# Optimization experiments

Hardware: AMD Instinct MI355X
Metric: run time of the kernel (lower is better)

Reference implementation:

```python
import jax, jax.numpy as jnp
import numpy as np

D_MODEL = 512
NHEAD = 8
DK = D_MODEL // NHEAD
DIM_FF = 2048
LN_EPS = 1e-5


def setup_inputs() -> dict:
    key = jax.random.key(0)
    ks = jax.random.split(key, 12)
    B, L = 8, 1024
    s = 1.0 / np.sqrt(D_MODEL)
    sf = 1.0 / np.sqrt(DIM_FF)
    return {
        "x": jax.random.normal(ks[0], (B, L, D_MODEL), jnp.float32),
        "key_padding_mask": jnp.zeros((B, L), dtype=bool),
        "bias": jax.random.normal(ks[1], (B, L, L), jnp.float32),
        # projection weights stored [in, out] so y = x @ W + b (matches torch Linear math)
        "Wq": jax.random.normal(ks[2], (D_MODEL, D_MODEL), jnp.float32) * s,
        "bq": jnp.zeros((D_MODEL,), jnp.float32),
        "Wk": jax.random.normal(ks[3], (D_MODEL, D_MODEL), jnp.float32) * s,
        "bk": jnp.zeros((D_MODEL,), jnp.float32),
        "Wv": jax.random.normal(ks[4], (D_MODEL, D_MODEL), jnp.float32) * s,
        "bv": jnp.zeros((D_MODEL,), jnp.float32),
        "Wo": jax.random.normal(ks[5], (D_MODEL, D_MODEL), jnp.float32) * s,
        "bo": jnp.zeros((D_MODEL,), jnp.float32),
        "ln1_g": jnp.ones((D_MODEL,), jnp.float32),
        "ln1_b": jnp.zeros((D_MODEL,), jnp.float32),
        "W1": jax.random.normal(ks[6], (D_MODEL, DIM_FF), jnp.float32) * s,
        "b1": jnp.zeros((DIM_FF,), jnp.float32),
        "W2": jax.random.normal(ks[7], (DIM_FF, D_MODEL), jnp.float32) * sf,
        "b2": jnp.zeros((D_MODEL,), jnp.float32),
        "ln2_g": jnp.ones((D_MODEL,), jnp.float32),
        "ln2_b": jnp.zeros((D_MODEL,), jnp.float32),
    }


def _layernorm(x, g, b):
    mu = jnp.mean(x, axis=-1, keepdims=True)
    var = jnp.mean(jnp.square(x - mu), axis=-1, keepdims=True)
    return (x - mu) * jax.lax.rsqrt(var + LN_EPS) * g + b


def reference(x, key_padding_mask, bias, Wq, bq, Wk, bk, Wv, bv, Wo, bo,
              ln1_g, ln1_b, W1, b1, W2, b2, ln2_g, ln2_b):
    B, L, H = x.shape
    residual = x
    # [B, L, D] -> [B, nhead, L, dk]
    q = (x @ Wq + bq).reshape(B, L, NHEAD, DK).transpose(0, 2, 1, 3)
    k = (x @ Wk + bk).reshape(B, L, NHEAD, DK).transpose(0, 2, 1, 3)
    v = (x @ Wv + bv).reshape(B, L, NHEAD, DK).transpose(0, 2, 1, 3)
    scores = jnp.einsum("bhqd,bhkd->bhqk", q, k) / np.sqrt(DK)
    scores = scores + bias[:, None, :, :]
    scores = jnp.where(key_padding_mask[:, None, None, :], -jnp.inf, scores)
    attn = jax.nn.softmax(scores, axis=-1)  # dropout p=0 (eval)
    out = jnp.einsum("bhqk,bhkd->bhqd", attn, v)
    out = out.transpose(0, 2, 1, 3).reshape(B, L, H)
    out = out @ Wo + bo
    x = _layernorm(residual + out, ln1_g, ln1_b)
    residual = x
    h = jax.nn.relu(x @ W1 + b1)
    x = h @ W2 + b2
    return _layernorm(residual + x, ln2_g, ln2_b)
```

## Files before the change

### kernel.cpp

```cpp
#include <hip/hip_runtime.h>
#include <math.h>

#define NHEAD 8
#define DKD 64
#define DMODEL 512
#define LSEQ 1024
#define NBL 8192

typedef __attribute__((ext_vector_type(8))) short bf8;
typedef __attribute__((ext_vector_type(4))) float f4;

__device__ inline unsigned short f2bf(float f) {
    union { float f; unsigned u; } v; v.f = f;
    unsigned r = v.u + 0x7FFFu + ((v.u >> 16) & 1u);
    return (unsigned short)(r >> 16);
}

__device__ __forceinline__ void gload16(const void* g, void* l) {
    __builtin_amdgcn_global_load_lds(
        (const __attribute__((address_space(1))) unsigned int*)g,
        (__attribute__((address_space(3))) unsigned int*)l, 16, 0, 0);
}

__global__ __launch_bounds__(256) void conv_bf16(
    const float* __restrict__ in, unsigned short* __restrict__ out, int n)
{
    int i = (blockIdx.x * 256 + threadIdx.x) * 4;
    if (i >= n) return;
    float4 v = *(const float4*)(in + i);
    ushort4 o;
    o.x = f2bf(v.x); o.y = f2bf(v.y); o.z = f2bf(v.z); o.w = f2bf(v.w);
    *(ushort4*)(out + i) = o;
}

__global__ __launch_bounds__(256) void transpose_bf16(
    const float* __restrict__ W, unsigned short* __restrict__ Wt, int K, int N)
{
    __shared__ float tile[64][65];
    const int k0 = blockIdx.y * 64, n0 = blockIdx.x * 64;
    const int c = threadIdx.x & 63, r0 = (threadIdx.x >> 6) * 16;
    #pragma unroll
    for (int i = 0; i < 16; ++i)
        tile[r0 + i][c] = W[(size_t)(k0 + r0 + i) * N + n0 + c];
    __syncthreads();
    #pragma unroll
    for (int i = 0; i < 16; ++i)
        Wt[(size_t)(n0 + r0 + i) * K + k0 + c] = f2bf(tile[c][r0 + i]);
}

__global__ void concat3(const float* __restrict__ a, const float* __restrict__ b,
                        const float* __restrict__ c, float* __restrict__ o)
{
    int i = blockIdx.x * 256 + threadIdx.x;
    if (i < 512) o[i] = a[i];
    else if (i < 1024) o[i] = b[i - 512];
    else if (i < 1536) o[i] = c[i - 1024];
}

__global__ void maskf_kernel(const unsigned char* __restrict__ m,
                             float* __restrict__ o, int n)
{
    int i = blockIdx.x * 256 + threadIdx.x;
    if (i < n) o[i] = m[i] ? -1e30f : 0.f;
}

__global__ __launch_bounds__(256) void mfma_gemm(
    const unsigned short* __restrict__ A, const unsigned short* __restrict__ Bt,
    const float* __restrict__ bias, const float* __restrict__ resid,
    void* __restrict__ outp, int M, int N, int K, int relu, int outmode,
    unsigned short* __restrict__ qs, unsigned short* __restrict__ ks,
    unsigned short* __restrict__ vts)
{
    __shared__ uint4 As[1024];
    __shared__ uint4 Bs[1024];

    const int t = threadIdx.x;
    const int lane = t & 63, w = t >> 6;
    const int g = lane >> 4, r15 = lane & 15;
    const int wr = w >> 1, wc = w & 1;
    const int rowBase = blockIdx.y * 128, colBase = blockIdx.x * 128;

    f4 acc[4][4] = {};

    const int r  = t >> 3;
    const int chs = (t & 7) ^ (r & 7);
    unsigned short* Al = (unsigned short*)As + (w * 8) * 64;
    unsigned short* Bl = (unsigned short*)Bs + (w * 8) * 64;

    for (int k0 = 0; k0 < K; k0 += 64) {
        __syncthreads();
        {
            const unsigned short* Ag = A  + (size_t)(rowBase + r) * K + k0 + chs * 8;
            const unsigned short* Bg = Bt + (size_t)(colBase + r) * K + k0 + chs * 8;
            #pragma unroll
            for (int p = 0; p < 4; ++p) {
                gload16(Ag + (size_t)(p * 32) * K, Al + p * 32 * 64);
                gload16(Bg + (size_t)(p * 32) * K, Bl + p * 32 * 64);
            }
        }
        __syncthreads();
        #pragma unroll
        for (int kk = 0; kk < 2; ++kk) {
            bf8 af[4], bfr[4];
            #pragma unroll
            for (int m = 0; m < 4; ++m) {
                int ra = wr * 64 + m * 16 + r15;
                af[m] = *(const bf8*)&As[ra * 8 + ((kk * 4 + g) ^ (ra & 7))];
                int rb = wc * 64 + m * 16 + r15;
                bfr[m] = *(const bf8*)&Bs[rb * 8 + ((kk * 4 + g) ^ (rb & 7))];
            }
            #pragma unroll
            for (int m = 0; m < 4; ++m)
                #pragma unroll
                for (int n = 0; n < 4; ++n)
                    acc[m][n] = __builtin_amdgcn_mfma_f32_16x16x32_bf16(
                        af[m], bfr[n], acc[m][n], 0, 0, 0);
        }
    }

    #pragma unroll
    for (int m = 0; m < 4; ++m) {
        #pragma unroll
        for (int n = 0; n < 4; ++n) {
            int col = colBase + wc * 64 + n * 16 + r15;
            float bv = bias[col];
            #pragma unroll
            for (int rr = 0; rr < 4; ++rr) {
                int row = rowBase + wr * 64 + m * 16 + g * 4 + rr;
                float v = acc[m][n][rr] + bv;
                if (relu) v = fmaxf(v, 0.f);
                if (outmode == 0) {
                    size_t idx = (size_t)row * N + col;
                    if (resid) v += resid[idx];
                    ((float*)outp)[idx] = v;
                } else if (outmode == 1) {
                    ((unsigned short*)outp)[(size_t)row * N + col] = f2bf(v);
                } else {
                    int sel = col >> 9, hd = col & 511;
                    int h = hd >> 6, dk = hd & 63;
                    int b = row >> 10, l = row & 1023;
                    unsigned short bw = f2bf(v);
                    size_t bh = (size_t)(b * NHEAD + h);
                    if (sel == 0)      qs[(bh * LSEQ + l) * DKD + dk] = bw;
                    else if (sel == 1) ks[(bh * LSEQ + l) * DKD + dk] = bw;
                    else               vts[(bh * DKD + dk) * LSEQ + l] = bw;
                }
            }
        }
    }
}

__global__ __launch_bounds__(256) void attn_mfma(
    const unsigned short* __restrict__ Qg, const unsigned short* __restrict__ Kg,
    const unsigned short* __restrict__ Vtg, const float* __restrict__ bias,
    const float* __restrict__ maskF, unsigned short* __restrict__ Ob)
{
    __shared__ uint4 Ks[512];
    __shared__ uint4 Vs[512];
    __shared__ unsigned int Pb[2048];

    const int t = threadIdx.x;
    const int lane = t & 63, w = t >> 6;
    const int g = lane >> 4, r15 = lane & 15;

    const int p = blockIdx.x;
    const int logical = (p & 7) * 128 + (p >> 3);
    const int bh = logical >> 4, qt = logical & 15;
    const int b = bh >> 3, h = bh & 7;

    bf8 qf[2];
    const int qrow = qt * 64 + w * 16 + r15;
    {
        const unsigned short* qp = Qg + ((size_t)bh * LSEQ + qrow) * DKD + g * 8;
        qf[0] = *(const bf8*)qp;
        qf[1] = *(const bf8*)(qp + 32);
    }

    float mrun = -1e30f, lsum = 0.f;
    f4 oacc[4] = {};

    const float* biasRow = bias + ((size_t)b << 20) + (size_t)qrow * LSEQ;
    const float* maskFb  = maskF + b * LSEQ;

    const int sr  = t >> 3;
    const int chs = (t & 7) ^ (sr & 7);
    unsigned short* Kl = (unsigned short*)Ks + (w * 8) * 64;
    unsigned short* Vl = (unsigned short*)Vs + (w * 8) * 64;
    unsigned short* Pw = (unsigned short*)&Pb[w * 512];

    for (int kt = 0; kt < 16; ++kt) {
        const int key0 = kt * 64;
        __syncthreads();
        {
            const unsigned short* Kgp = Kg  + ((size_t)bh * LSEQ + key0 + sr) * DKD + chs * 8;
            const unsigned short* Vgp = Vtg + ((size_t)bh * DKD + sr) * LSEQ + key0 + chs * 8;
            gload16(Kgp, Kl);
            gload16(Kgp + (size_t)32 * DKD, Kl + 32 * 64);
            gload16(Vgp, Vl);
            gload16(Vgp + (size_t)32 * LSEQ, Vl + 32 * 64);
        }
        __syncthreads();

        f4 sacc[4] = {};
        #pragma unroll
        for (int kk = 0; kk < 2; ++kk)
            #pragma unroll
            for (int m = 0; m < 4; ++m) {
                int row = m * 16 + r15;
                bf8 kf = *(const bf8*)&Ks[row * 8 + ((kk * 4 + g) ^ (row & 7))];
                sacc[m] = __builtin_amdgcn_mfma_f32_16x16x32_bf16(kf, qf[kk], sacc[m], 0, 0, 0);
            }

        float s[16];
        float pmax = -1e30f;
        #pragma unroll
        for (int m = 0; m < 4; ++m) {
            float4 bv = *(const float4*)(biasRow + key0 + m * 16 + g * 4);
            float4 mv = *(const float4*)(maskFb  + key0 + m * 16 + g * 4);
            const float* bvp = (const float*)&bv;
            const float* mvp = (const float*)&mv;
            #pragma unroll
            for (int j = 0; j < 4; ++j) {
                float sv = fmaf(sacc[m][j], 0.125f, bvp[j] + mvp[j]);
                s[m * 4 + j] = sv;
                pmax = fmaxf(pmax, sv);
            }
        }
        pmax = fmaxf(pmax, __shfl_xor(pmax, 16));
        pmax = fmaxf(pmax, __shfl_xor(pmax, 32));

        if (!__all(pmax <= mrun + 8.f)) {
            float mnew = fmaxf(mrun, pmax);
            float scale = __expf(mrun - mnew);
            lsum *= scale;
            #pragma unroll
            for (int m = 0; m < 4; ++m)
                #pragma unroll
                for (int j = 0; j < 4; ++j) oacc[m][j] *= scale;
            mrun = mnew;
        }

        float psum = 0.f;
        #pragma unroll
        for (int i = 0; i < 16; ++i) { s[i] = __expf(s[i] - mrun); psum += s[i]; }
        psum += __shfl_xor(psum, 16);
        psum += __shfl_xor(psum, 32);
        lsum += psum;

        #pragma unroll
        for (int m = 0; m < 4; ++m) {
            uint2 pk;
            pk.x = (unsigned)f2bf(s[m * 4 + 0]) | ((unsigned)f2bf(s[m * 4 + 1]) << 16);
            pk.y = (unsigned)f2bf(s[m * 4 + 2]) | ((unsigned)f2bf(s[m * 4 + 3]) << 16);
            int off = (r15 * 128 + m * 32 + g * 8) ^ ((r15 & 7) << 4);
            *(uint2*)((char*)Pw + off) = pk;
        }

        #pragma unroll
        for (int kk = 0; kk < 2; ++kk) {
            int off = (r15 * 128 + kk * 64 + g * 16) ^ ((r15 & 7) << 4);
            bf8 pf = *(const bf8*)((char*)Pw + off);
            #pragma unroll
            for (int m = 0; m < 4; ++m) {
                int row = m * 16 + r15;
                bf8 vf = *(const bf8*)&Vs[row * 8 + ((kk * 4 + g) ^ (row & 7))];
                oacc[m] = __builtin_amdgcn_mfma_f32_16x16x32_bf16(vf, pf, oacc[m], 0, 0, 0);
            }
        }
    }

    {
        float inv = 1.f / lsum;
        unsigned short* op = Ob + ((size_t)b * LSEQ + qrow) * DMODEL + h * DKD;
        #pragma unroll
        for (int m = 0; m < 4; ++m) {
            ushort4 o4;
            o4.x = f2bf(oacc[m][0] * inv);
            o4.y = f2bf(oacc[m][1] * inv);
            o4.z = f2bf(oacc[m][2] * inv);
            o4.w = f2bf(oacc[m][3] * inv);
            *(ushort4*)(op + m * 16 + g * 4) = o4;
        }
    }
}

__global__ __launch_bounds__(256) void ln_kernel(
    const float* __restrict__ in, const float* __restrict__ g,
    const float* __restrict__ bt, float* __restrict__ out,
    unsigned short* __restrict__ outb)
{
    const int row  = blockIdx.x * 4 + (threadIdx.x >> 6);
    const int lane = threadIdx.x & 63;
    const float* rp = in + (size_t)row * DMODEL + lane * 8;
    float4 x0 = *(const float4*)rp;
    float4 x1 = *(const float4*)(rp + 4);
    float xs[8] = {x0.x, x0.y, x0.z, x0.w, x1.x, x1.y, x1.z, x1.w};

    float sum = 0.f;
    #pragma unroll
    for (int i = 0; i < 8; ++i) sum += xs[i];
    #pragma unroll
    for (int off = 32; off; off >>= 1) sum += __shfl_xor(sum, off);
    float mu = sum * (1.f / 512.f);

    float vs = 0.f;
    #pragma unroll
    for (int i = 0; i < 8; ++i) { float d = xs[i] - mu; vs += d * d; }
    #pragma unroll
    for (int off = 32; off; off >>= 1) vs += __shfl_xor(vs, off);
    float rs = rsqrtf(vs * (1.f / 512.f) + 1e-5f);

    const float* gp = g  + lane * 8;
    const float* bp = bt + lane * 8;
    float4 g0 = *(const float4*)gp, g1 = *(const float4*)(gp + 4);
    float4 b0 = *(const float4*)bp, b1 = *(const float4*)(bp + 4);
    float gs[8] = {g0.x, g0.y, g0.z, g0.w, g1.x, g1.y, g1.z, g1.w};
    float bs[8] = {b0.x, b0.y, b0.z, b0.w, b1.x, b1.y, b1.z, b1.w};

    float res[8];
    #pragma unroll
    for (int i = 0; i < 8; ++i) res[i] = (xs[i] - mu) * rs * gs[i] + bs[i];

    float* op = out + (size_t)row * DMODEL + lane * 8;
    float4 r0 = {res[0], res[1], res[2], res[3]};
    float4 r1 = {res[4], res[5], res[6], res[7]};
    *(float4*)op       = r0;
    *(float4*)(op + 4) = r1;

    if (outb) {
        unsigned short* ob = outb + (size_t)row * DMODEL + lane * 8;
        ushort4 u0, u1;
        u0.x = f2bf(res[0]); u0.y = f2bf(res[1]); u0.z = f2bf(res[2]); u0.w = f2bf(res[3]);
        u1.x = f2bf(res[4]); u1.y = f2bf(res[5]); u1.z = f2bf(res[6]); u1.w = f2bf(res[7]);
        *(ushort4*)ob       = u0;
        *(ushort4*)(ob + 4) = u1;
    }
}

extern "C" void kernel_launch(void* const* d_in, const int* in_sizes, int n_in,
                              void* d_out, int out_size, void* d_ws, size_t ws_size,
                              hipStream_t stream)
{
    const float*         x    = (const float*)d_in[0];
    const unsigned char* mask = (const unsigned char*)d_in[1];
    const float*         bias = (const float*)d_in[2];
    const float* Wq = (const float*)d_in[3];
    const float* bq = (const float*)d_in[4];
    const float* Wk = (const float*)d_in[5];
    const float* bk = (const float*)d_in[6];
    const float* Wv = (const float*)d_in[7];
    const float* bv = (const float*)d_in[8];
    const float* Wo = (const float*)d_in[9];
    const float* bo = (const float*)d_in[10];
    const float* ln1g = (const float*)d_in[11];
    const float* ln1b = (const float*)d_in[12];
    const float* W1 = (const float*)d_in[13];
    const float* b1 = (const float*)d_in[14];
    const float* W2 = (const float*)d_in[15];
    const float* b2 = (const float*)d_in[16];
    const float* ln2g = (const float*)d_in[17];
    const float* ln2b = (const float*)d_in[18];

    char* W = (char*)d_ws;
    unsigned short* Qb   = (unsigned short*)(W);
    unsigned short* Kb   = (unsigned short*)(W + (8u << 20));
    unsigned short* Vtb  = (unsigned short*)(W + (16u << 20));
    unsigned short* Oball= (unsigned short*)(W + (24u << 20));
    unsigned short* hb   = (unsigned short*)(W);
    float*          y12  = (float*)(W + (32u << 20));
    float*          x1   = (float*)(W + (48u << 20));
    unsigned short* xb   = (unsigned short*)(W + (64u << 20));
    unsigned short* x1b  = xb;
    unsigned short* Wqkv = (unsigned short*)(W + (72u << 20));
    unsigned short* Wot  = (unsigned short*)(W + (74u << 20));
    unsigned short* W1t  = (unsigned short*)(W + (75u << 20));
    unsigned short* W2t  = (unsigned short*)(W + (77u << 20));
    float*          bqkv = (float*)(W + (79u << 20));
    float*          maskF= (float*)(W + (79u << 20) + 65536);
    float*          outp = (float*)d_out;

    conv_bf16<<<dim3(4096), dim3(256), 0, stream>>>(x, xb, NBL * DMODEL);
    transpose_bf16<<<dim3(8, 8),  dim3(256), 0, stream>>>(Wq, Wqkv,          512, 512);
    transpose_bf16<<<dim3(8, 8),  dim3(256), 0, stream>>>(Wk, Wqkv + 262144, 512, 512);
    transpose_bf16<<<dim3(8, 8),  dim3(256), 0, stream>>>(Wv, Wqkv + 524288, 512, 512);
    transpose_bf16<<<dim3(8, 8),  dim3(256), 0, stream>>>(Wo, Wot, 512, 512);
    transpose_bf16<<<dim3(32, 8), dim3(256), 0, stream>>>(W1, W1t, 512, 2048);
    transpose_bf16<<<dim3(8, 32), dim3(256), 0, stream>>>(W2, W2t, 2048, 512);
    concat3<<<dim3(6), dim3(256), 0, stream>>>(bq, bk, bv, bqkv);
    maskf_kernel<<<dim3(32), dim3(256), 0, stream>>>(mask, maskF, NBL);

    mfma_gemm<<<dim3(12, 64), dim3(256), 0, stream>>>(
        xb, Wqkv, bqkv, nullptr, nullptr, NBL, 1536, 512, 0, 2, Qb, Kb, Vtb);

    attn_mfma<<<dim3(1024), dim3(256), 0, stream>>>(Qb, Kb, Vtb, bias, maskF, Oball);

    mfma_gemm<<<dim3(4, 64), dim3(256), 0, stream>>>(
        Oball, Wot, bo, x, y12, NBL, 512, 512, 0, 0, nullptr, nullptr, nullptr);

    ln_kernel<<<dim3(NBL / 4), dim3(256), 0, stream>>>(y12, ln1g, ln1b, x1, x1b);

    mfma_gemm<<<dim3(16, 64), dim3(256), 0, stream>>>(
        x1b, W1t, b1, nullptr, hb, NBL, 2048, 512, 1, 1, nullptr, nullptr, nullptr);

    mfma_gemm<<<dim3(4, 64), dim3(256), 0, stream>>>(
        hb, W2t, b2, x1, y12, NBL, 512, 2048, 0, 0, nullptr, nullptr, nullptr);

    ln_kernel<<<dim3(NBL / 4), dim3(256), 0, stream>>>(y12, ln2g, ln2b, outp, nullptr);
}
```

Before: 386.7 us.

## Double-buffer attention with 128-query tiles, fuse prep kernels, narrow N=512 GEMM tiles

Attention now handles 128 query rows per block, two 16-row groups per wave, so K/V tiles are reused across twice as many queries. It double-buffers the K/V loads so the next tile's fetch overlaps current compute, and packs probabilities with v_cvt_pk_bf16_f32. The weight transposes and bias concat are merged into one launch. A new pass writes a mask-folded copy of the attention bias, so attention reads one array instead of bias plus mask, at the cost of an extra 32MB read and write. The GEMM is templated on tile width, and the N=512 GEMMs use 64-wide tiles to double the block count.

```diff
diff --git a/kernel.cpp b/kernel.cpp
--- a/kernel.cpp
+++ b/kernel.cpp
@@ -14,6 +14,12 @@
     union { float f; unsigned u; } v; v.f = f;
     unsigned r = v.u + 0x7FFFu + ((v.u >> 16) & 1u);
     return (unsigned short)(r >> 16);
+}
+
+__device__ __forceinline__ unsigned cvtpk(float lo, float hi) {
+    unsigned r;
+    asm("v_cvt_pk_bf16_f32 %0, %1, %2" : "=v"(r) : "v"(lo), "v"(hi));
+    return r;
 }
 
 __device__ __forceinline__ void gload16(const void* g, void* l) {
@@ -33,11 +39,29 @@
     *(ushort4*)(out + i) = o;
 }
 
-__global__ __launch_bounds__(256) void transpose_bf16(
-    const float* __restrict__ W, unsigned short* __restrict__ Wt, int K, int N)
+__global__ __launch_bounds__(256) void biasm_kernel(
+    const float* __restrict__ bias, const unsigned char* __restrict__ mask,
+    float* __restrict__ o)
+{
+    int i = blockIdx.x * 256 + threadIdx.x;
+    int flat = i * 4;
+    int b = flat >> 20;
+    int k = flat & 1023;
+    float4 v = ((const float4*)bias)[i];
+    uchar4 mk = *(const uchar4*)(mask + b * 1024 + k);
+    if (mk.x) v.x = -1e30f;
+    if (mk.y) v.y = -1e30f;
+    if (mk.z) v.z = -1e30f;
+    if (mk.w) v.w = -1e30f;
+    ((float4*)o)[i] = v;
+}
+
+__device__ __forceinline__ void do_transpose(
+    const float* __restrict__ W, unsigned short* __restrict__ Wt,
+    int K, int N, int bx, int by)
 {
     __shared__ float tile[64][65];
-    const int k0 = blockIdx.y * 64, n0 = blockIdx.x * 64;
+    const int k0 = by * 64, n0 = bx * 64;
     const int c = threadIdx.x & 63, r0 = (threadIdx.x >> 6) * 16;
     #pragma unroll
     for (int i = 0; i < 16; ++i)
@@ -48,22 +72,36 @@
         Wt[(size_t)(n0 + r0 + i) * K + k0 + c] = f2bf(tile[c][r0 + i]);
 }
 
-__global__ void concat3(const float* __restrict__ a, const float* __restrict__ b,
-                        const float* __restrict__ c, float* __restrict__ o)
-{
-    int i = blockIdx.x * 256 + threadIdx.x;
-    if (i < 512) o[i] = a[i];
-    else if (i < 1024) o[i] = b[i - 512];
-    else if (i < 1536) o[i] = c[i - 1024];
-}
-
-__global__ void maskf_kernel(const unsigned char* __restrict__ m,
-                             float* __restrict__ o, int n)
-{
-    int i = blockIdx.x * 256 + threadIdx.x;
-    if (i < n) o[i] = m[i] ? -1e30f : 0.f;
-}
-
+__global__ __launch_bounds__(256) void prep_weights(
+    const float* __restrict__ Wq, const float* __restrict__ Wk,
+    const float* __restrict__ Wv, const float* __restrict__ Wo,
+    const float* __restrict__ W1, const float* __restrict__ W2,
+    const float* __restrict__ bq, const float* __restrict__ bk,
+    const float* __restrict__ bv,
+    unsigned short* __restrict__ Wqkv, unsigned short* __restrict__ Wot,
+    unsigned short* __restrict__ W1t, unsigned short* __restrict__ W2t,
+    float* __restrict__ bqkv)
+{
+    int j = blockIdx.x;
+    if (j < 256) {
+        int which = j >> 6, tt = j & 63;
+        const float* src = which == 0 ? Wq : which == 1 ? Wk : which == 2 ? Wv : Wo;
+        unsigned short* dst = which == 0 ? Wqkv : which == 1 ? (Wqkv + 262144)
+                            : which == 2 ? (Wqkv + 524288) : Wot;
+        do_transpose(src, dst, 512, 512, tt & 7, tt >> 3);
+    } else if (j < 512) {
+        int tt = j - 256;
+        do_transpose(W1, W1t, 512, 2048, tt & 31, tt >> 5);
+    } else if (j < 768) {
+        int tt = j - 512;
+        do_transpose(W2, W2t, 2048, 512, tt & 7, tt >> 3);
+    } else {
+        for (int c = threadIdx.x; c < 1536; c += 256)
+            bqkv[c] = c < 512 ? bq[c] : c < 1024 ? bk[c - 512] : bv[c - 1024];
+    }
+}
+
+template<int BN>
 __global__ __launch_bounds__(256) void mfma_gemm(
     const unsigned short* __restrict__ A, const unsigned short* __restrict__ Bt,
     const float* __restrict__ bias, const float* __restrict__ resid,
@@ -72,17 +110,18 @@
     unsigned short* __restrict__ vts)
 {
     __shared__ uint4 As[1024];
-    __shared__ uint4 Bs[1024];
+    __shared__ uint4 Bs[BN * 8];
+    constexpr int NB = BN / 32;
 
     const int t = threadIdx.x;
     const int lane = t & 63, w = t >> 6;
     const int g = lane >> 4, r15 = lane & 15;
     const int wr = w >> 1, wc = w & 1;
-    const int rowBase = blockIdx.y * 128, colBase = blockIdx.x * 128;
-
-    f4 acc[4][4] = {};
-
-    const int r  = t >> 3;
+    const int rowBase = blockIdx.y * 128, colBase = blockIdx.x * BN;
+
+    f4 acc[4][NB] = {};
+
+    const int r   = t >> 3;
     const int chs = (t & 7) ^ (r & 7);
     unsigned short* Al = (unsigned short*)As + (w * 8) * 64;
     unsigned short* Bl = (unsigned short*)Bs + (w * 8) * 64;
@@ -93,26 +132,30 @@
             const unsigned short* Ag = A  + (size_t)(rowBase + r) * K + k0 + chs * 8;
             const unsigned short* Bg = Bt + (size_t)(colBase + r) * K + k0 + chs * 8;
             #pragma unroll
-            for (int p = 0; p < 4; ++p) {
+            for (int p = 0; p < 4; ++p)
                 gload16(Ag + (size_t)(p * 32) * K, Al + p * 32 * 64);
+            #pragma unroll
+            for (int p = 0; p < BN / 32; ++p)
                 gload16(Bg + (size_t)(p * 32) * K, Bl + p * 32 * 64);
-            }
         }
         __syncthreads();
         #pragma unroll
         for (int kk = 0; kk < 2; ++kk) {
-            bf8 af[4], bfr[4];
+            bf8 af[4], bfr[NB];
             #pragma unroll
             for (int m = 0; m < 4; ++m) {
                 int ra = wr * 64 + m * 16 + r15;
                 af[m] = *(const bf8*)&As[ra * 8 + ((kk * 4 + g) ^ (ra & 7))];
-                int rb = wc * 64 + m * 16 + r15;
-                bfr[m] = *(const bf8*)&Bs[rb * 8 + ((kk * 4 + g) ^ (rb & 7))];
+            }
+            #pragma unroll
+            for (int n = 0; n < NB; ++n) {
+                int rb = wc * (BN / 2) + n * 16 + r15;
+                bfr[n] = *(const bf8*)&Bs[rb * 8 + ((kk * 4 + g) ^ (rb & 7))];
             }
             #pragma unroll
             for (int m = 0; m < 4; ++m)
                 #pragma unroll
-                for (int n = 0; n < 4; ++n)
+                for (int n = 0; n < NB; ++n)
                     acc[m][n] = __builtin_amdgcn_mfma_f32_16x16x32_bf16(
                         af[m], bfr[n], acc[m][n], 0, 0, 0);
         }
@@ -121,8 +164,8 @@
     #pragma unroll
     for (int m = 0; m < 4; ++m) {
         #pragma unroll
-        for (int n = 0; n < 4; ++n) {
-            int col = colBase + wc * 64 + n * 16 + r15;
+        for (int n = 0; n < NB; ++n) {
+            int col = colBase + wc * (BN / 2) + n * 16 + r15;
             float bv = bias[col];
             #pragma unroll
             for (int rr = 0; rr < 4; ++rr) {
@@ -152,133 +195,157 @@
 
 __global__ __launch_bounds__(256) void attn_mfma(
     const unsigned short* __restrict__ Qg, const unsigned short* __restrict__ Kg,
-    const unsigned short* __restrict__ Vtg, const float* __restrict__ bias,
-    const float* __restrict__ maskF, unsigned short* __restrict__ Ob)
-{
-    __shared__ uint4 Ks[512];
-    __shared__ uint4 Vs[512];
-    __shared__ unsigned int Pb[2048];
+    const unsigned short* __restrict__ Vtg, const float* __restrict__ biasM,
+    unsigned short* __restrict__ Ob)
+{
+    __shared__ uint4 Ks[2][512];
+    __shared__ uint4 Vs[2][512];
+    __shared__ unsigned int Pb[4096];
 
     const int t = threadIdx.x;
     const int lane = t & 63, w = t >> 6;
     const int g = lane >> 4, r15 = lane & 15;
 
     const int p = blockIdx.x;
-    const int logical = (p & 7) * 128 + (p >> 3);
-    const int bh = logical >> 4, qt = logical & 15;
+    const int logical = (p & 7) * 64 + (p >> 3);
+    const int bh = logical >> 3, qt = logical & 7;
     const int b = bh >> 3, h = bh & 7;
-
-    bf8 qf[2];
-    const int qrow = qt * 64 + w * 16 + r15;
-    {
-        const unsigned short* qp = Qg + ((size_t)bh * LSEQ + qrow) * DKD + g * 8;
-        qf[0] = *(const bf8*)qp;
-        qf[1] = *(const bf8*)(qp + 32);
-    }
-
-    float mrun = -1e30f, lsum = 0.f;
-    f4 oacc[4] = {};
-
-    const float* biasRow = bias + ((size_t)b << 20) + (size_t)qrow * LSEQ;
-    const float* maskFb  = maskF + b * LSEQ;
+    const int qbase = qt * 128 + w * 32;
+
+    bf8 qf[2][2];
+    #pragma unroll
+    for (int u = 0; u < 2; ++u) {
+        const unsigned short* qp = Qg + ((size_t)bh * LSEQ + qbase + u * 16 + r15) * DKD + g * 8;
+        qf[u][0] = *(const bf8*)qp;
+        qf[u][1] = *(const bf8*)(qp + 32);
+    }
+
+    float mrun[2] = {-1e30f, -1e30f}, lsum[2] = {0.f, 0.f};
+    f4 oacc[2][4] = {};
 
     const int sr  = t >> 3;
     const int chs = (t & 7) ^ (sr & 7);
-    unsigned short* Kl = (unsigned short*)Ks + (w * 8) * 64;
-    unsigned short* Vl = (unsigned short*)Vs + (w * 8) * 64;
-    unsigned short* Pw = (unsigned short*)&Pb[w * 512];
+    unsigned int* Pw = Pb + w * 1024;
+
+    const size_t kBase = (size_t)bh * LSEQ * DKD;
+    const size_t vBase = (size_t)bh * DKD * LSEQ;
+
+    {
+        const unsigned short* Kgp = Kg  + kBase + (size_t)sr * DKD + chs * 8;
+        const unsigned short* Vgp = Vtg + vBase + (size_t)sr * LSEQ + chs * 8;
+        unsigned short* Kl = (unsigned short*)Ks[0] + (w * 8) * 64;
+        unsigned short* Vl = (unsigned short*)Vs[0] + (w * 8) * 64;
+        gload16(Kgp, Kl);
+        gload16(Kgp + (size_t)32 * DKD, Kl + 32 * 64);
+        gload16(Vgp, Vl);
+        gload16(Vgp + (size_t)32 * LSEQ, Vl + 32 * 64);
+    }
+    __syncthreads();
 
     for (int kt = 0; kt < 16; ++kt) {
+        const int cur = kt & 1;
         const int key0 = kt * 64;
-        __syncthreads();
-        {
-            const unsigned short* Kgp = Kg  + ((size_t)bh * LSEQ + key0 + sr) * DKD + chs * 8;
-            const unsigned short* Vgp = Vtg + ((size_t)bh * DKD + sr) * LSEQ + key0 + chs * 8;
+        if (kt < 15) {
+            const int nk0 = key0 + 64;
+            const unsigned short* Kgp = Kg  + kBase + (size_t)(nk0 + sr) * DKD + chs * 8;
+            const unsigned short* Vgp = Vtg + vBase + (size_t)sr * LSEQ + nk0 + chs * 8;
+            unsigned short* Kl = (unsigned short*)Ks[cur ^ 1] + (w * 8) * 64;
+            unsigned short* Vl = (unsigned short*)Vs[cur ^ 1] + (w * 8) * 64;
             gload16(Kgp, Kl);
             gload16(Kgp + (size_t)32 * DKD, Kl + 32 * 64);
             gload16(Vgp, Vl);
             gload16(Vgp + (size_t)32 * LSEQ, Vl + 32 * 64);
         }
-        __syncthreads();
-
-        f4 sacc[4] = {};
+
+        f4 sacc[2][4] = {};
         #pragma unroll
         for (int kk = 0; kk < 2; ++kk)
             #pragma unroll
             for (int m = 0; m < 4; ++m) {
                 int row = m * 16 + r15;
-                bf8 kf = *(const bf8*)&Ks[row * 8 + ((kk * 4 + g) ^ (row & 7))];
-                sacc[m] = __builtin_amdgcn_mfma_f32_16x16x32_bf16(kf, qf[kk], sacc[m], 0, 0, 0);
-            }
-
-        float s[16];
-        float pmax = -1e30f;
-        #pragma unroll
-        for (int m = 0; m < 4; ++m) {
-            float4 bv = *(const float4*)(biasRow + key0 + m * 16 + g * 4);
-            float4 mv = *(const float4*)(maskFb  + key0 + m * 16 + g * 4);
-            const float* bvp = (const float*)&bv;
-            const float* mvp = (const float*)&mv;
-            #pragma unroll
-            for (int j = 0; j < 4; ++j) {
-                float sv = fmaf(sacc[m][j], 0.125f, bvp[j] + mvp[j]);
-                s[m * 4 + j] = sv;
-                pmax = fmaxf(pmax, sv);
-            }
-        }
-        pmax = fmaxf(pmax, __shfl_xor(pmax, 16));
-        pmax = fmaxf(pmax, __shfl_xor(pmax, 32));
-
-        if (!__all(pmax <= mrun + 8.f)) {
-            float mnew = fmaxf(mrun, pmax);
-            float scale = __expf(mrun - mnew);
-            lsum *= scale;
-            #pragma unroll
-            for (int m = 0; m < 4; ++m)
+                bf8 kf = *(const bf8*)&Ks[cur][row * 8 + ((kk * 4 + g) ^ (row & 7))];
+                sacc[0][m] = __builtin_amdgcn_mfma_f32_16x16x32_bf16(kf, qf[0][kk], sacc[0][m], 0, 0, 0);
+                sacc[1][m] = __builtin_amdgcn_mfma_f32_16x16x32_bf16(kf, qf[1][kk], sacc[1][m], 0, 0, 0);
+            }
+
+        #pragma unroll
+        for (int u = 0; u < 2; ++u) {
+            const float* biasRow = biasM + ((size_t)b << 20)
+                                 + (size_t)(qbase + u * 16 + r15) * LSEQ + key0;
+            float s[16];
+            float pmax = -1e30f;
+            #pragma unroll
+            for (int m = 0; m < 4; ++m) {
+                float4 bv = *(const float4*)(biasRow + m * 16 + g * 4);
+                const float* bvp = (const float*)&bv;
                 #pragma unroll
-                for (int j = 0; j < 4; ++j) oacc[m][j] *= scale;
-            mrun = mnew;
-        }
-
-        float psum = 0.f;
-        #pragma unroll
-        for (int i = 0; i < 16; ++i) { s[i] = __expf(s[i] - mrun); psum += s[i]; }
-        psum += __shfl_xor(psum, 16);
-        psum += __shfl_xor(psum, 32);
-        lsum += psum;
-
-        #pragma unroll
-        for (int m = 0; m < 4; ++m) {
-            uint2 pk;
-            pk.x = (unsigned)f2bf(s[m * 4 + 0]) | ((unsigned)f2bf(s[m * 4 + 1]) << 16);
-            pk.y = (unsigned)f2bf(s[m * 4 + 2]) | ((unsigned)f2bf(s[m * 4 + 3]) << 16);
-            int off = (r15 * 128 + m * 32 + g * 8) ^ ((r15 & 7) << 4);
-            *(uint2*)((char*)Pw + off) = pk;
+                for (int j = 0; j < 4; ++j) {
+                    float sv = fmaf(sacc[u][m][j], 0.125f, bvp[j]);
+                    s[m * 4 + j] = sv;
+                    pmax = fmaxf(pmax, sv);
+                }
+            }
+            pmax = fmaxf(pmax, __shfl_xor(pmax, 16));
+            pmax = fmaxf(pmax, __shfl_xor(pmax, 32));
+
+            if (!__all(pmax <= mrun[u] + 8.f)) {
+                float mnew = fmaxf(mrun[u], pmax);
+                float scale = __expf(mrun[u] - mnew);
+                lsum[u] *= scale;
+                #pragma unroll
+                for (int m = 0; m < 4; ++m)
+                    #pragma unroll
+                    for (int j = 0; j < 4; ++j) oacc[u][m][j] *= scale;
+                mrun[u] = mnew;
+            }
+
+            float psum = 0.f;
+            #pragma unroll
+            for (int i = 0; i < 16; ++i) { s[i] = __expf(s[i] - mrun[u]); psum += s[i]; }
+            psum += __shfl_xor(psum, 16);
+            psum += __shfl_xor(psum, 32);
+            lsum[u] += psum;
+
+            #pragma unroll
+            for (int m = 0; m < 4; ++m) {
+                uint2 pk;
+                pk.x = cvtpk(s[m * 4 + 0], s[m * 4 + 1]);
+                pk.y = cvtpk(s[m * 4 + 2], s[m * 4 + 3]);
+                int off = ((u * 16 + r15) * 128 + m * 32 + g * 8) ^ ((r15 & 7) << 4);
+                *(uint2*)((char*)Pw + off) = pk;
+            }
         }
 
         #pragma unroll
         for (int kk = 0; kk < 2; ++kk) {
-            int off = (r15 * 128 + kk * 64 + g * 16) ^ ((r15 & 7) << 4);
-            bf8 pf = *(const bf8*)((char*)Pw + off);
+            bf8 pf[2];
+            #pragma unroll
+            for (int u = 0; u < 2; ++u) {
+                int off = ((u * 16 + r15) * 128 + kk * 64 + g * 16) ^ ((r15 & 7) << 4);
+                pf[u] = *(const bf8*)((char*)Pw + off);
+            }
             #pragma unroll
             for (int m = 0; m < 4; ++m) {
                 int row = m * 16 + r15;
-                bf8 vf = *(const bf8*)&Vs[row * 8 + ((kk * 4 + g) ^ (row & 7))];
-                oacc[m] = __builtin_amdgcn_mfma_f32_16x16x32_bf16(vf, pf, oacc[m], 0, 0, 0);
-            }
-        }
-    }
-
-    {
-        float inv = 1.f / lsum;
-        unsigned short* op = Ob + ((size_t)b * LSEQ + qrow) * DMODEL + h * DKD;
+                bf8 vf = *(const bf8*)&Vs[cur][row * 8 + ((kk * 4 + g) ^ (row & 7))];
+                oacc[0][m] = __builtin_amdgcn_mfma_f32_16x16x32_bf16(vf, pf[0], oacc[0][m], 0, 0, 0);
+                oacc[1][m] = __builtin_amdgcn_mfma_f32_16x16x32_bf16(vf, pf[1], oacc[1][m], 0, 0, 0);
+            }
+        }
+        __syncthreads();
+    }
+
+    #pragma unroll
+    for (int u = 0; u < 2; ++u) {
+        float inv = 1.f / lsum[u];
+        unsigned short* op = Ob + ((size_t)b * LSEQ + qbase + u * 16 + r15) * DMODEL + h * DKD;
         #pragma unroll
         for (int m = 0; m < 4; ++m) {
             ushort4 o4;
-            o4.x = f2bf(oacc[m][0] * inv);
-            o4.y = f2bf(oacc[m][1] * inv);
-            o4.z = f2bf(oacc[m][2] * inv);
-            o4.w = f2bf(oacc[m][3] * inv);
+            o4.x = f2bf(oacc[u][m][0] * inv);
+            o4.y = f2bf(oacc[u][m][1] * inv);
+            o4.z = f2bf(oacc[u][m][2] * inv);
+            o4.w = f2bf(oacc[u][m][3] * inv);
             *(ushort4*)(op + m * 16 + g * 4) = o4;
         }
     }
@@ -367,42 +434,37 @@
     unsigned short* Vtb  = (unsigned short*)(W + (16u << 20));
     unsigned short* Oball= (unsigned short*)(W + (24u << 20));
     unsigned short* hb   = (unsigned short*)(W);
+    float*          biasM= (float*)(W + (32u << 20));
     float*          y12  = (float*)(W + (32u << 20));
     float*          x1   = (float*)(W + (48u << 20));
-    unsigned short* xb   = (unsigned short*)(W + (64u << 20));
+    unsigned short* xb   = (unsigned short*)(W + (66u << 20));
     unsigned short* x1b  = xb;
-    unsigned short* Wqkv = (unsigned short*)(W + (72u << 20));
-    unsigned short* Wot  = (unsigned short*)(W + (74u << 20));
-    unsigned short* W1t  = (unsigned short*)(W + (75u << 20));
-    unsigned short* W2t  = (unsigned short*)(W + (77u << 20));
-    float*          bqkv = (float*)(W + (79u << 20));
-    float*          maskF= (float*)(W + (79u << 20) + 65536);
+    unsigned short* Wqkv = (unsigned short*)(W + (74u << 20));
+    unsigned short* Wot  = (unsigned short*)(W + (76u << 20));
+    unsigned short* W1t  = (unsigned short*)(W + (77u << 20));
+    unsigned short* W2t  = (unsigned short*)(W + (79u << 20));
+    float*          bqkv = (float*)(W + (81u << 20));
     float*          outp = (float*)d_out;
 
     conv_bf16<<<dim3(4096), dim3(256), 0, stream>>>(x, xb, NBL * DMODEL);
-    transpose_bf16<<<dim3(8, 8),  dim3(256), 0, stream>>>(Wq, Wqkv,          512, 512);
-    transpose_bf16<<<dim3(8, 8),  dim3(256), 0, stream>>>(Wk, Wqkv + 262144, 512, 512);
-    transpose_bf16<<<dim3(8, 8),  dim3(256), 0, stream>>>(Wv, Wqkv + 524288, 512, 512);
-    transpose_bf16<<<dim3(8, 8),  dim3(256), 0, stream>>>(Wo, Wot, 512, 512);
-    transpose_bf16<<<dim3(32, 8), dim3(256), 0, stream>>>(W1, W1t, 512, 2048);
-    transpose_bf16<<<dim3(8, 32), dim3(256), 0, stream>>>(W2, W2t, 2048, 512);
-    concat3<<<dim3(6), dim3(256), 0, stream>>>(bq, bk, bv, bqkv);
-    maskf_kernel<<<dim3(32), dim3(256), 0, stream>>>(mask, maskF, NBL);
-
-    mfma_gemm<<<dim3(12, 64), dim3(256), 0, stream>>>(
+    prep_weights<<<dim3(769), dim3(256), 0, stream>>>(
+        Wq, Wk, Wv, Wo, W1, W2, bq, bk, bv, Wqkv, Wot, W1t, W2t, bqkv);
+    biasm_kernel<<<dim3(8192), dim3(256), 0, stream>>>(bias, mask, biasM);
+
+    mfma_gemm<128><<<dim3(12, 64), dim3(256), 0, stream>>>(
         xb, Wqkv, bqkv, nullptr, nullptr, NBL, 1536, 512, 0, 2, Qb, Kb, Vtb);
 
-    attn_mfma<<<dim3(1024), dim3(256), 0, stream>>>(Qb, Kb, Vtb, bias, maskF, Oball);
-
-    mfma_gemm<<<dim3(4, 64), dim3(256), 0, stream>>>(
+    attn_mfma<<<dim3(512), dim3(256), 0, stream>>>(Qb, Kb, Vtb, biasM, Oball);
+
+    mfma_gemm<64><<<dim3(8, 64), dim3(256), 0, stream>>>(
         Oball, Wot, bo, x, y12, NBL, 512, 512, 0, 0, nullptr, nullptr, nullptr);
 
     ln_kernel<<<dim3(NBL / 4), dim3(256), 0, stream>>>(y12, ln1g, ln1b, x1, x1b);
 
-    mfma_gemm<<<dim3(16, 64), dim3(256), 0, stream>>>(
+    mfma_gemm<128><<<dim3(16, 64), dim3(256), 0, stream>>>(
         x1b, W1t, b1, nullptr, hb, NBL, 2048, 512, 1, 1, nullptr, nullptr, nullptr);
 
-    mfma_gemm<<<dim3(4, 64), dim3(256), 0, stream>>>(
+    mfma_gemm<64><<<dim3(8, 64), dim3(256), 0, stream>>>(
         hb, W2t, b2, x1, y12, NBL, 512, 2048, 0, 0, nullptr, nullptr, nullptr);
 
     ln_kernel<<<dim3(NBL / 4), dim3(256), 0, stream>>>(y12, ln2g, ln2b, outp, nullptr);
```

New measurement: 358.4 us. 1.08x faster.
